# Kernel tuning notes

Hardware: AMD Instinct MI355X
Metric: run time of the kernel (lower is better)

The kernel has to match this reference:

```python
import jax, jax.numpy as jnp
import numpy as np

HIDDEN_DIM = 512  # H; hidden/encoder feature dim is 2H = 1024


def setup_inputs() -> dict:
    key = jax.random.key(0)
    k1, k2, k3, k4, k5 = jax.random.split(key, 5)
    B, S, D2, H = 16, 4096, 2 * HIDDEN_DIM, HIDDEN_DIM
    hidden = jax.random.normal(k1, (B, D2), dtype=jnp.float32)
    encoder_outputs = jax.random.normal(k2, (B, S, D2), dtype=jnp.float32)
    # nn.Linear(4H, H): weight [H, 4H] in torch; store transposed [4H, H] for x @ W
    W_attn = jax.random.normal(k3, (2 * D2, H), dtype=jnp.float32) * (1.0 / np.sqrt(2 * D2))
    b_attn = jax.random.normal(k4, (H,), dtype=jnp.float32) * 0.01
    # nn.Linear(H, 1, bias=False): weight [1, H] -> vector [H]
    w_v = jax.random.normal(k5, (H,), dtype=jnp.float32) * (1.0 / np.sqrt(H))
    return {"hidden": hidden, "encoder_outputs": encoder_outputs,
            "W_attn": W_attn, "b_attn": b_attn, "w_v": w_v}


def reference(hidden, encoder_outputs, W_attn, b_attn, w_v):
    B, S, D2 = encoder_outputs.shape
    # Broadcast decoder hidden over seq positions and concat with encoder outputs.
    hid = jnp.broadcast_to(hidden[:, None, :], (B, S, D2))
    cat = jnp.concatenate([hid, encoder_outputs], axis=2)        # [B, S, 4H]
    energy = jnp.tanh(cat @ W_attn + b_attn)                      # [B, S, H]
    scores = jnp.einsum('bsh,h->bs', energy, w_v)                 # [B, S]
    attention = jax.nn.softmax(scores, axis=1)                    # [B, S]
    context = jnp.einsum('bs,bsd->bd', attention, encoder_outputs)  # [B, 2H]
    return context
```

## Files before the change

### kernel.cpp

```cpp
#include <hip/hip_runtime.h>
#include <hip/hip_bf16.h>
#include <math.h>

#define HD   512
#define D2   1024
#define SEQ  4096
#define BAT  16
#define BM   64
#define BN   256
#define BK   32

typedef _Float16 half8 __attribute__((ext_vector_type(8)));
typedef float    f32x4 __attribute__((ext_vector_type(4)));
typedef __attribute__((address_space(3))) void lds_void_t;
typedef __attribute__((address_space(1))) void glb_void_t;

__global__ void wconv_kernel(const float* __restrict__ W, _Float16* __restrict__ WtS) {
  __shared__ float tile[32][17];
  const int kt  = blockIdx.x;
  const int nbg = blockIdx.y;
  const int nh  = nbg >> 4, nbl = nbg & 15;
  const int t   = threadIdx.x;
  {
    const int n16 = t & 15, kk = t >> 4;
    #pragma unroll
    for (int i = 0; i < 2; ++i) {
      const int k = kk + i * 16;
      tile[k][n16] = W[(size_t)(D2 + kt * 32 + k) * HD + nh * 256 + nbl * 16 + n16];
    }
  }
  __syncthreads();
  if (t < 64) {
    const int kc = t >> 4, nlo = t & 15;
    half8 h;
    #pragma unroll
    for (int j = 0; j < 8; ++j) h[j] = (_Float16)tile[kc * 8 + j][nlo];
    *(half8*)(WtS + ((size_t)(kt * 2 + nh) * 1024 + nbl * 64 + kc * 16 + nlo) * 8) = h;
  }
}

__global__ void hproj_kernel(const float* __restrict__ hidden,
                             const float* __restrict__ W,
                             float* __restrict__ hproj) {
  const int b  = blockIdx.x >> 3;
  const int kc = blockIdx.x & 7;
  const int h  = threadIdx.x;
  float a0 = 0.f, a1 = 0.f;
  #pragma unroll 4
  for (int i = 0; i < 128; ++i) {
    const int d = kc * 128 + i;
    const float hd = hidden[b * D2 + d];
    a0 += hd * W[(size_t)d * HD + h];
    a1 += hd * W[(size_t)d * HD + h + 256];
  }
  atomicAdd(&hproj[b * HD + h], a0);
  atomicAdd(&hproj[b * HD + h + 256], a1);
}

__global__ __launch_bounds__(256, 4) void scores_kernel(
    const float* __restrict__ enc, const _Float16* __restrict__ WtS,
    const float* __restrict__ hproj, const float* __restrict__ b_attn,
    const float* __restrict__ w_v, float* __restrict__ scores)
{
  __shared__ __align__(16) _Float16 As[2][BM * BK];
  __shared__ __align__(16) _Float16 Bs[2][BN * BK];

  const int s0  = blockIdx.x * BM;
  const int nh  = blockIdx.y;
  const int b   = blockIdx.z;
  const int tid = threadIdx.x, lane = tid & 63, w = tid >> 6;
  const int col = lane & 15, quad = lane >> 4;
  const int strip = w >> 1, nq2 = w & 1;

  const float* encB = enc + ((size_t)b * SEQ + s0) * D2;
  const _Float16* WtB = WtS + (size_t)nh * 1024 * 8;

  const int arow = tid >> 2, akc = tid & 3;
  const float* aSrcBase = encB + (size_t)arow * D2 + akc * 8;
  const int aDstOff = (akc * 64 + (arow ^ (akc << 2))) * 8;
  const int a0off = (quad * 64 + ((strip * 32 + col)      ^ (quad << 2))) * 8;
  const int a1off = (quad * 64 + ((strip * 32 + 16 + col) ^ (quad << 2))) * 8;

  f32x4 acc0[8], acc1[8];
  const f32x4 z = {0.f, 0.f, 0.f, 0.f};
  #pragma unroll
  for (int i = 0; i < 8; ++i) { acc0[i] = z; acc1[i] = z; }

  f32x4 Ra0, Ra1, Rb0, Rb1;

  auto loadA = [&](int kt, f32x4& v0, f32x4& v1) {
    const float* p = aSrcBase + kt * BK;
    v0 = *(const f32x4*)p;
    v1 = *(const f32x4*)(p + 4);
  };
  auto storeA = [&](int buf, const f32x4& v0, const f32x4& v1) {
    half8 h;
    h[0] = (_Float16)v0[0]; h[1] = (_Float16)v0[1];
    h[2] = (_Float16)v0[2]; h[3] = (_Float16)v0[3];
    h[4] = (_Float16)v1[0]; h[5] = (_Float16)v1[1];
    h[6] = (_Float16)v1[2]; h[7] = (_Float16)v1[3];
    *(half8*)&As[buf][aDstOff] = h;
  };
  auto issueB = [&](int kt, int buf) {
    #pragma unroll
    for (int i = 0; i < 4; ++i) {
      const int c = i * 256 + tid;
      __builtin_amdgcn_global_load_lds(
          (glb_void_t*)(WtB + (size_t)kt * 16384 + c * 8),
          (lds_void_t*)((char*)&Bs[buf][0] + c * 16), 16, 0, 0);
    }
  };
  auto compute = [&](int buf) {
    half8 a0 = *(const half8*)&As[buf][a0off];
    half8 a1 = *(const half8*)&As[buf][a1off];
    #pragma unroll
    for (int nt = 0; nt < 8; ++nt) {
      const int nbl_local = nq2 * 8 + nt;
      half8 bf = *(const half8*)&Bs[buf][(nbl_local * 64 + quad * 16 + col) * 8];
      acc0[nt] = __builtin_amdgcn_mfma_f32_16x16x32_f16(a0, bf, acc0[nt], 0, 0, 0);
      acc1[nt] = __builtin_amdgcn_mfma_f32_16x16x32_f16(a1, bf, acc1[nt], 0, 0, 0);
    }
  };

  loadA(0, Ra0, Ra1);
  storeA(0, Ra0, Ra1);
  issueB(0, 0);
  loadA(1, Rb0, Rb1);
  __syncthreads();

  #pragma unroll 2
  for (int kt = 0; kt < 32; ++kt) {
    const int cur = kt & 1, nxt = cur ^ 1;
    if (kt + 1 < 32) issueB(kt + 1, nxt);
    if (kt + 2 < 32) {
      if (kt & 1) loadA(kt + 2, Rb0, Rb1);
      else        loadA(kt + 2, Ra0, Ra1);
    }
    compute(cur);
    if (kt + 1 < 32) {
      if (kt & 1) storeA(nxt, Ra0, Ra1);
      else        storeA(nxt, Rb0, Rb1);
    }
    __syncthreads();
  }

  float p0[4] = {0.f, 0.f, 0.f, 0.f}, p1[4] = {0.f, 0.f, 0.f, 0.f};
  const float* hp = hproj + b * HD + nh * 256;
  #pragma unroll
  for (int nt = 0; nt < 8; ++nt) {
    const int nl = nq2 * 128 + nt * 16 + col;
    const float hb = hp[nl] + b_attn[nh * 256 + nl];
    const float wv = w_v[nh * 256 + nl];
    #pragma unroll
    for (int r = 0; r < 4; ++r) {
      {
        float x = fminf(fmaxf(acc0[nt][r] + hb, -15.f), 15.f);
        float ex = __expf(2.f * x);
        p0[r] += wv * __fdividef(ex - 1.f, ex + 1.f);
      }
      {
        float x = fminf(fmaxf(acc1[nt][r] + hb, -15.f), 15.f);
        float ex = __expf(2.f * x);
        p1[r] += wv * __fdividef(ex - 1.f, ex + 1.f);
      }
    }
  }
  #pragma unroll
  for (int off = 8; off >= 1; off >>= 1) {
    #pragma unroll
    for (int r = 0; r < 4; ++r) {
      p0[r] += __shfl_xor(p0[r], off, 64);
      p1[r] += __shfl_xor(p1[r], off, 64);
    }
  }
  if (col == 0) {
    const int m0 = s0 + strip * 32 + quad * 4;
    #pragma unroll
    for (int r = 0; r < 4; ++r) {
      atomicAdd(&scores[b * SEQ + m0 + r], p0[r]);
      atomicAdd(&scores[b * SEQ + m0 + 16 + r], p1[r]);
    }
  }
}

__global__ void softmax_kernel(float* __restrict__ scores) {
  const int b = blockIdx.x;
  float* sc = scores + b * SEQ;
  __shared__ float red[16];
  const int tid = threadIdx.x;
  float loc[16];
  float mx = -1e30f;
  #pragma unroll
  for (int i = 0; i < 16; ++i) { loc[i] = sc[i * 256 + tid]; mx = fmaxf(mx, loc[i]); }
  #pragma unroll
  for (int off = 32; off >= 1; off >>= 1) mx = fmaxf(mx, __shfl_xor(mx, off, 64));
  if ((tid & 63) == 0) red[tid >> 6] = mx;
  __syncthreads();
  mx = fmaxf(fmaxf(red[0], red[1]), fmaxf(red[2], red[3]));
  float sum = 0.f;
  #pragma unroll
  for (int i = 0; i < 16; ++i) { loc[i] = __expf(loc[i] - mx); sum += loc[i]; }
  #pragma unroll
  for (int off = 32; off >= 1; off >>= 1) sum += __shfl_xor(sum, off, 64);
  if ((tid & 63) == 0) red[8 + (tid >> 6)] = sum;
  __syncthreads();
  sum = red[8] + red[9] + red[10] + red[11];
  const float inv = 1.0f / sum;
  #pragma unroll
  for (int i = 0; i < 16; ++i) sc[i * 256 + tid] = loc[i] * inv;
}

__global__ __launch_bounds__(256) void context_kernel(const float* __restrict__ attn,
                                                      const float* __restrict__ enc,
                                                      float* __restrict__ out) {
  const int b  = blockIdx.y;
  const int s0 = blockIdx.x * 64;
  const int tid = threadIdx.x;
  const float* encB = enc + ((size_t)b * SEQ + s0) * D2 + tid * 4;
  const float* at   = attn + b * SEQ + s0;
  f32x4 acc0 = {0.f, 0.f, 0.f, 0.f}, acc1 = {0.f, 0.f, 0.f, 0.f};
  #pragma unroll 8
  for (int i = 0; i < 64; i += 2) {
    acc0 += at[i]     * *(const f32x4*)(encB + (size_t)i * D2);
    acc1 += at[i + 1] * *(const f32x4*)(encB + (size_t)(i + 1) * D2);
  }
  f32x4 acc = acc0 + acc1;
  float* o = out + b * D2 + tid * 4;
  atomicAdd(o + 0, acc[0]);
  atomicAdd(o + 1, acc[1]);
  atomicAdd(o + 2, acc[2]);
  atomicAdd(o + 3, acc[3]);
}

extern "C" void kernel_launch(void* const* d_in, const int* in_sizes, int n_in,
                              void* d_out, int out_size, void* d_ws, size_t ws_size,
                              hipStream_t stream) {
  (void)in_sizes; (void)n_in; (void)ws_size;
  const float* hidden = (const float*)d_in[0];
  const float* enc    = (const float*)d_in[1];
  const float* W      = (const float*)d_in[2];
  const float* b_attn = (const float*)d_in[3];
  const float* w_v    = (const float*)d_in[4];
  float* out = (float*)d_out;

  char* ws = (char*)d_ws;
  _Float16* WtS = (_Float16*)ws;
  float* hproj  = (float*)(ws + (1 << 20));
  float* scores = (float*)(ws + (1 << 20) + 32768);

  hipMemsetAsync(d_out, 0, (size_t)out_size * sizeof(float), stream);
  hipMemsetAsync(hproj, 0, BAT * HD * sizeof(float), stream);
  hipMemsetAsync(scores, 0, (size_t)BAT * SEQ * sizeof(float), stream);

  wconv_kernel  <<<dim3(32, 32),            256, 0, stream>>>(W, WtS);
  hproj_kernel  <<<dim3(128),               256, 0, stream>>>(hidden, W, hproj);
  scores_kernel <<<dim3(SEQ / BM, 2, BAT),  256, 0, stream>>>(enc, WtS, hproj, b_attn, w_v, scores);
  softmax_kernel<<<dim3(BAT),               256, 0, stream>>>(scores);
  context_kernel<<<dim3(SEQ / 64, BAT),     256, 0, stream>>>(scores, enc, out);
}
```

Before: 491.8 us.

## Restructure scores GEMM with 32x32 MFMA, larger M tile, B read from global

The scores kernel grows the M tile from 64 to 128 rows and switches to 32x32x16 MFMA with a 2x2 warp layout. The B (weight) fragments are now loaded straight from global/L2 into registers, and only A is staged in LDS. The weight pre-conversion kernel is rewritten to emit a fragment-ordered layout with fewer blocks, and A uses a three-deep register prefetch. This cuts LDS traffic and block count and raises MFMA efficiency, but it relies on L2 hits for B and lowers occupancy to 2 blocks per CU.

```diff
diff --git a/kernel.cpp b/kernel.cpp
--- a/kernel.cpp
+++ b/kernel.cpp
@@ -6,36 +6,28 @@
 #define D2   1024
 #define SEQ  4096
 #define BAT  16
-#define BM   64
-#define BN   256
+#define BM   128
 #define BK   32
 
-typedef _Float16 half8 __attribute__((ext_vector_type(8)));
-typedef float    f32x4 __attribute__((ext_vector_type(4)));
-typedef __attribute__((address_space(3))) void lds_void_t;
-typedef __attribute__((address_space(1))) void glb_void_t;
+typedef _Float16 half8  __attribute__((ext_vector_type(8)));
+typedef float    f32x4  __attribute__((ext_vector_type(4)));
+typedef float    f32x16 __attribute__((ext_vector_type(16)));
 
 __global__ void wconv_kernel(const float* __restrict__ W, _Float16* __restrict__ WtS) {
-  __shared__ float tile[32][17];
-  const int kt  = blockIdx.x;
-  const int nbg = blockIdx.y;
-  const int nh  = nbg >> 4, nbl = nbg & 15;
-  const int t   = threadIdx.x;
-  {
-    const int n16 = t & 15, kk = t >> 4;
-    #pragma unroll
-    for (int i = 0; i < 2; ++i) {
-      const int k = kk + i * 16;
-      tile[k][n16] = W[(size_t)(D2 + kt * 32 + k) * HD + nh * 256 + nbl * 16 + n16];
-    }
-  }
-  __syncthreads();
-  if (t < 64) {
-    const int kc = t >> 4, nlo = t & 15;
+  const int kt = blockIdx.x;
+  const int nh = blockIdx.y;
+  const int t  = threadIdx.x;
+  #pragma unroll
+  for (int i = 0; i < 4; ++i) {
+    const int c   = i * 256 + t;
+    const int q   = c >> 9;
+    const int kh2 = (c >> 8) & 1;
+    const int n   = c & 255;
     half8 h;
     #pragma unroll
-    for (int j = 0; j < 8; ++j) h[j] = (_Float16)tile[kc * 8 + j][nlo];
-    *(half8*)(WtS + ((size_t)(kt * 2 + nh) * 1024 + nbl * 64 + kc * 16 + nlo) * 8) = h;
+    for (int j = 0; j < 8; ++j)
+      h[j] = (_Float16)W[(size_t)(D2 + kt * 32 + q * 16 + kh2 * 8 + j) * HD + nh * 256 + n];
+    *(half8*)(WtS + ((size_t)(((nh * 32 + kt) * 2 + q) * 2 + kh2) * 256 + n) * 8) = h;
   }
 }
 
@@ -57,129 +49,132 @@
   atomicAdd(&hproj[b * HD + h + 256], a1);
 }
 
-__global__ __launch_bounds__(256, 4) void scores_kernel(
+__global__ __launch_bounds__(256, 2) void scores_kernel(
     const float* __restrict__ enc, const _Float16* __restrict__ WtS,
     const float* __restrict__ hproj, const float* __restrict__ b_attn,
     const float* __restrict__ w_v, float* __restrict__ scores)
 {
-  __shared__ __align__(16) _Float16 As[2][BM * BK];
-  __shared__ __align__(16) _Float16 Bs[2][BN * BK];
-
-  const int s0  = blockIdx.x * BM;
-  const int nh  = blockIdx.y;
-  const int b   = blockIdx.z;
-  const int tid = threadIdx.x, lane = tid & 63, w = tid >> 6;
-  const int col = lane & 15, quad = lane >> 4;
-  const int strip = w >> 1, nq2 = w & 1;
+  __shared__ __align__(16) _Float16 As[2 * 4 * 128 * 8];
+
+  const int s0   = blockIdx.x * BM;
+  const int nh   = blockIdx.y;
+  const int b    = blockIdx.z;
+  const int tid  = threadIdx.x, lane = tid & 63, w = tid >> 6;
+  const int wy   = w >> 1, wx = w & 1;
+  const int llo  = lane & 31, lhi = lane >> 5;
 
   const float* encB = enc + ((size_t)b * SEQ + s0) * D2;
-  const _Float16* WtB = WtS + (size_t)nh * 1024 * 8;
-
-  const int arow = tid >> 2, akc = tid & 3;
-  const float* aSrcBase = encB + (size_t)arow * D2 + akc * 8;
-  const int aDstOff = (akc * 64 + (arow ^ (akc << 2))) * 8;
-  const int a0off = (quad * 64 + ((strip * 32 + col)      ^ (quad << 2))) * 8;
-  const int a1off = (quad * 64 + ((strip * 32 + 16 + col) ^ (quad << 2))) * 8;
-
-  f32x4 acc0[8], acc1[8];
-  const f32x4 z = {0.f, 0.f, 0.f, 0.f};
-  #pragma unroll
-  for (int i = 0; i < 8; ++i) { acc0[i] = z; acc1[i] = z; }
-
-  f32x4 Ra0, Ra1, Rb0, Rb1;
-
-  auto loadA = [&](int kt, f32x4& v0, f32x4& v1) {
-    const float* p = aSrcBase + kt * BK;
-    v0 = *(const f32x4*)p;
-    v1 = *(const f32x4*)(p + 4);
+
+  const int arow = tid >> 1, akc = tid & 1;
+  const float* aSrc = encB + (size_t)arow * D2 + akc * 16;
+
+  const _Float16* Bbase = WtS + (size_t)nh * 32 * 8192
+                        + lhi * 2048 + wx * 1024 + llo * 8;
+
+  int afOff[2][2];
+  #pragma unroll
+  for (int mi = 0; mi < 2; ++mi)
+    #pragma unroll
+    for (int q = 0; q < 2; ++q)
+      afOff[mi][q] = ((q * 2 + lhi) * 128 + wy * 64 + mi * 32 + llo) * 8;
+
+  f32x16 acc[2][4];
+  #pragma unroll
+  for (int mi = 0; mi < 2; ++mi)
+    #pragma unroll
+    for (int nf = 0; nf < 4; ++nf)
+      acc[mi][nf] = (f32x16)(0.f);
+
+  f32x4 R[2][4];
+
+  auto loadA = [&](int kt, f32x4* r) {
+    const float* p = aSrc + kt * BK;
+    r[0] = *(const f32x4*)(p);
+    r[1] = *(const f32x4*)(p + 4);
+    r[2] = *(const f32x4*)(p + 8);
+    r[3] = *(const f32x4*)(p + 12);
   };
-  auto storeA = [&](int buf, const f32x4& v0, const f32x4& v1) {
-    half8 h;
-    h[0] = (_Float16)v0[0]; h[1] = (_Float16)v0[1];
-    h[2] = (_Float16)v0[2]; h[3] = (_Float16)v0[3];
-    h[4] = (_Float16)v1[0]; h[5] = (_Float16)v1[1];
-    h[6] = (_Float16)v1[2]; h[7] = (_Float16)v1[3];
-    *(half8*)&As[buf][aDstOff] = h;
+  auto storeA = [&](int buf, const f32x4* r) {
+    half8 h0, h1;
+    #pragma unroll
+    for (int j = 0; j < 4; ++j) {
+      h0[j] = (_Float16)r[0][j]; h0[4 + j] = (_Float16)r[1][j];
+      h1[j] = (_Float16)r[2][j]; h1[4 + j] = (_Float16)r[3][j];
+    }
+    *(half8*)&As[((buf * 4 + akc * 2 + 0) * 128 + arow) * 8] = h0;
+    *(half8*)&As[((buf * 4 + akc * 2 + 1) * 128 + arow) * 8] = h1;
   };
-  auto issueB = [&](int kt, int buf) {
-    #pragma unroll
-    for (int i = 0; i < 4; ++i) {
-      const int c = i * 256 + tid;
-      __builtin_amdgcn_global_load_lds(
-          (glb_void_t*)(WtB + (size_t)kt * 16384 + c * 8),
-          (lds_void_t*)((char*)&Bs[buf][0] + c * 16), 16, 0, 0);
-    }
-  };
-  auto compute = [&](int buf) {
-    half8 a0 = *(const half8*)&As[buf][a0off];
-    half8 a1 = *(const half8*)&As[buf][a1off];
-    #pragma unroll
-    for (int nt = 0; nt < 8; ++nt) {
-      const int nbl_local = nq2 * 8 + nt;
-      half8 bf = *(const half8*)&Bs[buf][(nbl_local * 64 + quad * 16 + col) * 8];
-      acc0[nt] = __builtin_amdgcn_mfma_f32_16x16x32_f16(a0, bf, acc0[nt], 0, 0, 0);
-      acc1[nt] = __builtin_amdgcn_mfma_f32_16x16x32_f16(a1, bf, acc1[nt], 0, 0, 0);
-    }
-  };
-
-  loadA(0, Ra0, Ra1);
-  storeA(0, Ra0, Ra1);
-  issueB(0, 0);
-  loadA(1, Rb0, Rb1);
-  __syncthreads();
+
+  loadA(0, R[0]);
+  storeA(0, R[0]);
+  loadA(1, R[0]);
+  loadA(2, R[1]);
+  asm volatile("s_waitcnt lgkmcnt(0)\n\ts_barrier" ::: "memory");
 
   #pragma unroll 2
   for (int kt = 0; kt < 32; ++kt) {
     const int cur = kt & 1, nxt = cur ^ 1;
-    if (kt + 1 < 32) issueB(kt + 1, nxt);
-    if (kt + 2 < 32) {
-      if (kt & 1) loadA(kt + 2, Rb0, Rb1);
-      else        loadA(kt + 2, Ra0, Ra1);
-    }
-    compute(cur);
-    if (kt + 1 < 32) {
-      if (kt & 1) storeA(nxt, Ra0, Ra1);
-      else        storeA(nxt, Rb0, Rb1);
-    }
-    __syncthreads();
-  }
-
-  float p0[4] = {0.f, 0.f, 0.f, 0.f}, p1[4] = {0.f, 0.f, 0.f, 0.f};
-  const float* hp = hproj + b * HD + nh * 256;
-  #pragma unroll
-  for (int nt = 0; nt < 8; ++nt) {
-    const int nl = nq2 * 128 + nt * 16 + col;
-    const float hb = hp[nl] + b_attn[nh * 256 + nl];
-    const float wv = w_v[nh * 256 + nl];
-    #pragma unroll
-    for (int r = 0; r < 4; ++r) {
-      {
-        float x = fminf(fmaxf(acc0[nt][r] + hb, -15.f), 15.f);
+    const _Float16* Bkt = Bbase + (size_t)kt * 8192;
+    half8 bf[2][4];
+    #pragma unroll
+    for (int q = 0; q < 2; ++q)
+      #pragma unroll
+      for (int nf = 0; nf < 4; ++nf)
+        bf[q][nf] = *(const half8*)(Bkt + q * 4096 + nf * 256);
+    half8 af[2][2];
+    #pragma unroll
+    for (int mi = 0; mi < 2; ++mi)
+      #pragma unroll
+      for (int q = 0; q < 2; ++q)
+        af[mi][q] = *(const half8*)&As[(cur * 4 * 128) * 8 + afOff[mi][q]];
+    #pragma unroll
+    for (int nf = 0; nf < 4; ++nf)
+      #pragma unroll
+      for (int mi = 0; mi < 2; ++mi)
+        #pragma unroll
+        for (int q = 0; q < 2; ++q)
+          acc[mi][nf] = __builtin_amdgcn_mfma_f32_32x32x16_f16(af[mi][q], bf[q][nf], acc[mi][nf], 0, 0, 0);
+    if (kt + 1 < 32) storeA(nxt, R[kt & 1]);
+    if (kt + 3 < 32) loadA(kt + 3, R[kt & 1]);
+    asm volatile("s_waitcnt lgkmcnt(0)\n\ts_barrier" ::: "memory");
+  }
+
+  float p[2][16];
+  #pragma unroll
+  for (int mi = 0; mi < 2; ++mi)
+    #pragma unroll
+    for (int r = 0; r < 16; ++r) p[mi][r] = 0.f;
+
+  #pragma unroll
+  for (int nf = 0; nf < 4; ++nf) {
+    const int n = nh * 256 + wx * 128 + nf * 32 + llo;
+    const float hb = hproj[b * HD + n] + b_attn[n];
+    const float wv = w_v[n];
+    #pragma unroll
+    for (int mi = 0; mi < 2; ++mi)
+      #pragma unroll
+      for (int r = 0; r < 16; ++r) {
+        float x = fminf(fmaxf(acc[mi][nf][r] + hb, -15.f), 15.f);
         float ex = __expf(2.f * x);
-        p0[r] += wv * __fdividef(ex - 1.f, ex + 1.f);
+        p[mi][r] += wv * __fdividef(ex - 1.f, ex + 1.f);
       }
-      {
-        float x = fminf(fmaxf(acc1[nt][r] + hb, -15.f), 15.f);
-        float ex = __expf(2.f * x);
-        p1[r] += wv * __fdividef(ex - 1.f, ex + 1.f);
+  }
+  #pragma unroll
+  for (int off = 1; off <= 16; off <<= 1)
+    #pragma unroll
+    for (int mi = 0; mi < 2; ++mi)
+      #pragma unroll
+      for (int r = 0; r < 16; ++r)
+        p[mi][r] += __shfl_xor(p[mi][r], off, 64);
+
+  if (llo == 0) {
+    #pragma unroll
+    for (int mi = 0; mi < 2; ++mi)
+      #pragma unroll
+      for (int r = 0; r < 16; ++r) {
+        const int m = wy * 64 + mi * 32 + (r & 3) + 8 * (r >> 2) + 4 * lhi;
+        atomicAdd(&scores[b * SEQ + s0 + m], p[mi][r]);
       }
-    }
-  }
-  #pragma unroll
-  for (int off = 8; off >= 1; off >>= 1) {
-    #pragma unroll
-    for (int r = 0; r < 4; ++r) {
-      p0[r] += __shfl_xor(p0[r], off, 64);
-      p1[r] += __shfl_xor(p1[r], off, 64);
-    }
-  }
-  if (col == 0) {
-    const int m0 = s0 + strip * 32 + quad * 4;
-    #pragma unroll
-    for (int r = 0; r < 4; ++r) {
-      atomicAdd(&scores[b * SEQ + m0 + r], p0[r]);
-      atomicAdd(&scores[b * SEQ + m0 + 16 + r], p1[r]);
-    }
   }
 }
 
@@ -252,7 +247,7 @@
   hipMemsetAsync(hproj, 0, BAT * HD * sizeof(float), stream);
   hipMemsetAsync(scores, 0, (size_t)BAT * SEQ * sizeof(float), stream);
 
-  wconv_kernel  <<<dim3(32, 32),            256, 0, stream>>>(W, WtS);
+  wconv_kernel  <<<dim3(32, 2),             256, 0, stream>>>(W, WtS);
   hproj_kernel  <<<dim3(128),               256, 0, stream>>>(hidden, W, hproj);
   scores_kernel <<<dim3(SEQ / BM, 2, BAT),  256, 0, stream>>>(enc, WtS, hproj, b_attn, w_v, scores);
   softmax_kernel<<<dim3(BAT),               256, 0, stream>>>(scores);
```

After: 511.9 us. +4.1%, slower.
